# Optimization experiments

Measured on AMD Instinct MI355X. Metric: run time of the kernel, lower is better.

Reference implementation:

```python
import jax, jax.numpy as jnp
import numpy as np


def setup_inputs() -> dict:
    key = jax.random.key(0)
    k1, k2 = jax.random.split(key)
    enc_output = jax.random.normal(k1, (4, 4096, 1024), dtype=jnp.float32)
    dec_output = jax.random.normal(k2, (4, 4096, 1024), dtype=jnp.float32)
    return {"enc_output": enc_output, "dec_output": dec_output}


def reference(enc_output, dec_output):
    # a_t[b, e, t] = sum_d enc[b, e, d] * dec[b, t, d]   -> [B, T_enc, T_dec]
    a_t = jnp.einsum('bed,btd->bet', enc_output, dec_output)
    # softmax over dim=1 (the T_enc axis), no scaling, no mask (faithful to source)
    a_t = jax.nn.softmax(a_t, axis=1)
    # c_t[b, t, d] = sum_e a_t[b, e, t] * enc[b, e, d]   -> [B, T_dec, D]
    c_t = jnp.einsum('bet,bed->btd', a_t, enc_output)
    return c_t
```

## Files before the change

### kernel.cpp

```cpp
#include <hip/hip_runtime.h>
#include <hip/hip_fp16.h>

typedef _Float16 half_t;
typedef _Float16 f16x8 __attribute__((ext_vector_type(8)));
typedef _Float16 f16x4 __attribute__((ext_vector_type(4)));
typedef float f32x4 __attribute__((ext_vector_type(4)));
typedef __attribute__((address_space(3))) half_t* lds_p;

#define SEQ 4096
#define DDIM 1024
#define NBATCH 4

__device__ __forceinline__ void gload16(const half_t* g, half_t* l) {
  __builtin_amdgcn_global_load_lds((const __attribute__((address_space(1))) void*)g,
                                   (__attribute__((address_space(3))) void*)l, 16, 0, 0);
}

__device__ __forceinline__ f16x8 ds_read128(lds_p p) {
  f16x8 r;
  asm volatile("ds_read_b128 %0, %1" : "=v"(r) : "v"(p));
  return r;
}

__global__ __launch_bounds__(256) void conv_f16(const float* __restrict__ src,
                                                half_t* __restrict__ dst) {
  int i = blockIdx.x * 256 + threadIdx.x;
  float4 x = ((const float4*)src)[i];
  f16x4 o = {(half_t)x.x, (half_t)x.y, (half_t)x.z, (half_t)x.w};
  *(f16x4*)(dst + (size_t)i * 4) = o;
}

__global__ __launch_bounds__(256) void transconv_f16(const float* __restrict__ src,
                                                     half_t* __restrict__ dstF,
                                                     half_t* __restrict__ dstT) {
  __shared__ float tile[32][33];
  int b = blockIdx.z;
  int e0 = blockIdx.x * 32, d0 = blockIdx.y * 32;
  const float* s = src + (size_t)b * SEQ * DDIM;
  half_t* df = dstF + (size_t)b * SEQ * DDIM;
  half_t* dt = dstT + (size_t)b * DDIM * SEQ;
  int tx = threadIdx.x & 31, ty = threadIdx.x >> 5;
#pragma unroll
  for (int i = 0; i < 4; i++) {
    int e = e0 + ty + i * 8;
    float v = s[(size_t)e * DDIM + d0 + tx];
    tile[ty + i * 8][tx] = v;
    df[(size_t)e * DDIM + d0 + tx] = (half_t)v;
  }
  __syncthreads();
#pragma unroll
  for (int i = 0; i < 4; i++) {
    int d = d0 + ty + i * 8;
    dt[(size_t)d * SEQ + e0 + tx] = (half_t)tile[tx][ty + i * 8];
  }
}

#define TM 256
#define TN 256
#define TK 64

__global__ __launch_bounds__(512, 2) void gemm256_p2(const half_t* __restrict__ A,
                                                     const half_t* __restrict__ B,
                                                     float* __restrict__ C, int M, int N,
                                                     int K, int kc, long sA, long sB, long sC,
                                                     int atom) {
  A += (size_t)blockIdx.z * (size_t)sA;
  B += (size_t)blockIdx.z * (size_t)sB;
  C += (size_t)blockIdx.z * (size_t)sC;
  __shared__ __align__(16) half_t As[2][TM * TK];
  __shared__ __align__(16) half_t Bs[2][TN * TK];
  const int tid = threadIdx.x;
  const int wave = tid >> 6, lane = tid & 63;
  const int wm = (wave >> 2) * 128, wn = (wave & 3) * 64;
  const int mrow = lane & 15, quad = lane >> 4;

  f32x4 acc[8][4];
#pragma unroll
  for (int i = 0; i < 8; i++)
#pragma unroll
    for (int j = 0; j < 4; j++) acc[i][j] = {0.f, 0.f, 0.f, 0.f};

  const half_t* Ag = A + (size_t)(blockIdx.x * TM) * K;
  const half_t* Bg = B + (size_t)(blockIdx.y * TN) * K;
  lds_p As3 = (lds_p)&As[0][0];
  lds_p Bs3 = (lds_p)&Bs[0][0];

  auto stage = [&](int buf, int k0) {
#pragma unroll
    for (int i = 0; i < 4; i++) {
      int cid = i * 512 + tid;
      int row = cid >> 3, slot = cid & 7;
      int chunk = slot ^ (row & 7);
      gload16(Ag + (size_t)row * K + k0 + chunk * 8, &As[buf][row * TK + slot * 8]);
      gload16(Bg + (size_t)row * K + k0 + chunk * 8, &Bs[buf][row * TK + slot * 8]);
    }
  };

  const int nt = kc / TK;
  stage(0, 0);
  asm volatile("s_waitcnt vmcnt(0)" ::: "memory");
  __builtin_amdgcn_s_barrier();
  int cur = 0;
  for (int t = 0; t < nt; ++t) {
    if (t + 1 < nt) stage(cur ^ 1, (t + 1) * TK);
    lds_p Ab = As3 + cur * (TM * TK);
    lds_p Bb = Bs3 + cur * (TN * TK);
#pragma unroll
    for (int ks = 0; ks < 2; ks++) {
      f16x8 af[8], bf[4];
#pragma unroll
      for (int i = 0; i < 8; i++) {
        int ra = wm + i * 16 + mrow;
        int sa = (ks * 4 + quad) ^ (ra & 7);
        af[i] = ds_read128(Ab + ra * TK + sa * 8);
      }
#pragma unroll
      for (int j = 0; j < 4; j++) {
        int rb = wn + j * 16 + mrow;
        int sb = (ks * 4 + quad) ^ (rb & 7);
        bf[j] = ds_read128(Bb + rb * TK + sb * 8);
      }
      asm volatile("s_waitcnt lgkmcnt(0)" ::: "memory");
      __builtin_amdgcn_sched_barrier(0);
#pragma unroll
      for (int mi = 0; mi < 8; mi++)
#pragma unroll
        for (int ni = 0; ni < 4; ni++)
          acc[mi][ni] =
              __builtin_amdgcn_mfma_f32_16x16x32_f16(af[mi], bf[ni], acc[mi][ni], 0, 0, 0);
    }
    asm volatile("s_waitcnt vmcnt(0)" ::: "memory");
    __builtin_amdgcn_s_barrier();
    cur ^= 1;
  }
#pragma unroll
  for (int mi = 0; mi < 8; mi++) {
#pragma unroll
    for (int ni = 0; ni < 4; ni++) {
      int row0 = blockIdx.x * TM + wm + mi * 16 + quad * 4;
      int col = blockIdx.y * TN + wn + ni * 16 + mrow;
      float* Cp = C + (size_t)row0 * N + col;
      if (atom) {
#pragma unroll
        for (int r = 0; r < 4; r++) unsafeAtomicAdd(Cp + (size_t)r * N, acc[mi][ni][r]);
      } else {
#pragma unroll
        for (int r = 0; r < 4; r++) Cp[(size_t)r * N] = acc[mi][ni][r];
      }
    }
  }
}

__global__ __launch_bounds__(256) void softmax_rows(const float* __restrict__ S,
                                                    half_t* __restrict__ P) {
  const int row = blockIdx.x;
  const float4* Sr = (const float4*)(S + (size_t)row * SEQ);
  const int tid = threadIdx.x, lane = tid & 63, wave = tid >> 6;
  __shared__ float red[4];
  __shared__ float bc;
  float4 v[4];
  float m = -1e30f;
#pragma unroll
  for (int j = 0; j < 4; j++) {
    v[j] = Sr[tid + j * 256];
    m = fmaxf(m, fmaxf(fmaxf(v[j].x, v[j].y), fmaxf(v[j].z, v[j].w)));
  }
#pragma unroll
  for (int o = 32; o; o >>= 1) m = fmaxf(m, __shfl_xor(m, o));
  if (lane == 0) red[wave] = m;
  __syncthreads();
  if (tid == 0) bc = fmaxf(fmaxf(red[0], red[1]), fmaxf(red[2], red[3]));
  __syncthreads();
  m = bc;
  float s = 0.f;
#pragma unroll
  for (int j = 0; j < 4; j++) {
    v[j].x = __expf(v[j].x - m);
    v[j].y = __expf(v[j].y - m);
    v[j].z = __expf(v[j].z - m);
    v[j].w = __expf(v[j].w - m);
    s += v[j].x + v[j].y + v[j].z + v[j].w;
  }
#pragma unroll
  for (int o = 32; o; o >>= 1) s += __shfl_xor(s, o);
  __syncthreads();
  if (lane == 0) red[wave] = s;
  __syncthreads();
  if (tid == 0) bc = red[0] + red[1] + red[2] + red[3];
  __syncthreads();
  float r = 1.0f / bc;
  f16x4* Pr = (f16x4*)(P + (size_t)row * SEQ);
#pragma unroll
  for (int j = 0; j < 4; j++) {
    f16x4 o = {(half_t)(v[j].x * r), (half_t)(v[j].y * r), (half_t)(v[j].z * r),
               (half_t)(v[j].w * r)};
    Pr[tid + j * 256] = o;
  }
}

__global__ __launch_bounds__(256) void naive_attn(const float* __restrict__ enc,
                                                  const float* __restrict__ dec,
                                                  float* __restrict__ out) {
  const int b = blockIdx.y, t = blockIdx.x;
  const float* encb = enc + (size_t)b * SEQ * DDIM;
  const float* q = dec + ((size_t)b * SEQ + t) * DDIM;
  __shared__ float qs[DDIM];
  __shared__ float sc[SEQ];
  __shared__ float red[4];
  __shared__ float bc;
  const int tid = threadIdx.x, lane = tid & 63, wave = tid >> 6;
  for (int i = tid; i < DDIM; i += 256) qs[i] = q[i];
  __syncthreads();
  for (int e = tid; e < SEQ; e += 256) {
    const float* er = encb + (size_t)e * DDIM;
    float s = 0.f;
    for (int d = 0; d < DDIM; d += 4) {
      float4 ev = *(const float4*)(er + d);
      s += ev.x * qs[d] + ev.y * qs[d + 1] + ev.z * qs[d + 2] + ev.w * qs[d + 3];
    }
    sc[e] = s;
  }
  __syncthreads();
  float m = -1e30f;
  for (int e = tid; e < SEQ; e += 256) m = fmaxf(m, sc[e]);
#pragma unroll
  for (int o = 32; o; o >>= 1) m = fmaxf(m, __shfl_xor(m, o));
  if (lane == 0) red[wave] = m;
  __syncthreads();
  if (tid == 0) bc = fmaxf(fmaxf(red[0], red[1]), fmaxf(red[2], red[3]));
  __syncthreads();
  m = bc;
  float s = 0.f;
  for (int e = tid; e < SEQ; e += 256) {
    float p = __expf(sc[e] - m);
    sc[e] = p;
    s += p;
  }
#pragma unroll
  for (int o = 32; o; o >>= 1) s += __shfl_xor(s, o);
  __syncthreads();
  if (lane == 0) red[wave] = s;
  __syncthreads();
  if (tid == 0) bc = red[0] + red[1] + red[2] + red[3];
  __syncthreads();
  const float rinv = 1.0f / bc;
  const int d0 = tid * 4;
  float4 acc = {0.f, 0.f, 0.f, 0.f};
  for (int e = 0; e < SEQ; e++) {
    float p = sc[e];
    float4 ev = *(const float4*)(encb + (size_t)e * DDIM + d0);
    acc.x += p * ev.x;
    acc.y += p * ev.y;
    acc.z += p * ev.z;
    acc.w += p * ev.w;
  }
  float4* o4 = (float4*)(out + ((size_t)b * SEQ + t) * DDIM + d0);
  float4 res = {acc.x * rinv, acc.y * rinv, acc.z * rinv, acc.w * rinv};
  *o4 = res;
}

extern "C" void kernel_launch(void* const* d_in, const int* in_sizes, int n_in, void* d_out,
                              int out_size, void* d_ws, size_t ws_size, hipStream_t stream) {
  const float* enc = (const float*)d_in[0];
  const float* dec = (const float*)d_in[1];
  float* out = (float*)d_out;

  const size_t SZ_S = (size_t)SEQ * SEQ * 4;
  const size_t SZ_P = (size_t)SEQ * SEQ * 2;
  const size_t SZ_H = (size_t)NBATCH * SEQ * DDIM * 2;
  const size_t NEED = SZ_S + SZ_P + 3 * SZ_H;

  const int nconv = NBATCH * SEQ * DDIM / 4 / 256;

  if (ws_size >= NEED) {
    char* w = (char*)d_ws;
    float* S = (float*)w;
    half_t* P = (half_t*)(w + SZ_S);
    half_t* decF = (half_t*)(w + SZ_S + SZ_P);
    half_t* encF = (half_t*)(w + SZ_S + SZ_P + SZ_H);
    half_t* encT = (half_t*)(w + SZ_S + SZ_P + 2 * SZ_H);

    hipMemsetAsync(out, 0, (size_t)NBATCH * SEQ * DDIM * 4, stream);
    conv_f16<<<nconv, 256, 0, stream>>>(dec, decF);
    transconv_f16<<<dim3(SEQ / 32, DDIM / 32, NBATCH), 256, 0, stream>>>(enc, encF, encT);

    for (int b = 0; b < NBATCH; b++) {
      const size_t eo = (size_t)b * SEQ * DDIM;
      gemm256_p2<<<dim3(SEQ / TM, SEQ / TN, 1), 512, 0, stream>>>(
          decF + eo, encF + eo, S, SEQ, SEQ, DDIM, DDIM, 0, 0, 0, 0);
      softmax_rows<<<SEQ, 256, 0, stream>>>(S, P);
      gemm256_p2<<<dim3(SEQ / TM, DDIM / TN, 4), 512, 0, stream>>>(
          P, encT + (size_t)b * DDIM * SEQ, out + eo, SEQ, DDIM, SEQ, SEQ / 4, SEQ / 4,
          SEQ / 4, 0, 1);
    }
  } else {
    naive_attn<<<dim3(SEQ, NBATCH), 256, 0, stream>>>(enc, dec, out);
  }
}
```

Measured before the change: 682.1 us.

## Shrink GEMM N-tile to 128 and add triple-buffered LDS prefetch pipeline

The GEMM tile changes from 256x256 to 256x128 and the shared-memory staging goes from double to triple buffering. Loads for tile t+2 are issued while tile t is computed, with partial vmcnt waits so only the oldest stage has to land. The aim is to hide global-load latency and raise the number of blocks in the grid. In exchange, each wave does fewer MFMAs per byte loaded, which lowers data reuse. LDS use is 3x(32KB+16KB)=144KB per block, which may cut occupancy below the 2 blocks the launch bounds request.

```diff
diff --git a/kernel.cpp b/kernel.cpp
--- a/kernel.cpp
+++ b/kernel.cpp
@@ -56,29 +56,29 @@
 }
 
 #define TM 256
-#define TN 256
+#define TN 128
 #define TK 64
 
-__global__ __launch_bounds__(512, 2) void gemm256_p2(const half_t* __restrict__ A,
-                                                     const half_t* __restrict__ B,
-                                                     float* __restrict__ C, int M, int N,
-                                                     int K, int kc, long sA, long sB, long sC,
-                                                     int atom) {
+__global__ __launch_bounds__(512, 2) void gemm_p3(const half_t* __restrict__ A,
+                                                  const half_t* __restrict__ B,
+                                                  float* __restrict__ C, int M, int N, int K,
+                                                  int kc, long sA, long sB, long sC,
+                                                  int atom) {
   A += (size_t)blockIdx.z * (size_t)sA;
   B += (size_t)blockIdx.z * (size_t)sB;
   C += (size_t)blockIdx.z * (size_t)sC;
-  __shared__ __align__(16) half_t As[2][TM * TK];
-  __shared__ __align__(16) half_t Bs[2][TN * TK];
+  __shared__ __align__(16) half_t As[3][TM * TK];
+  __shared__ __align__(16) half_t Bs[3][TN * TK];
   const int tid = threadIdx.x;
   const int wave = tid >> 6, lane = tid & 63;
-  const int wm = (wave >> 2) * 128, wn = (wave & 3) * 64;
+  const int wm = (wave >> 2) * 128, wn = (wave & 3) * 32;
   const int mrow = lane & 15, quad = lane >> 4;
 
-  f32x4 acc[8][4];
+  f32x4 acc[8][2];
 #pragma unroll
   for (int i = 0; i < 8; i++)
 #pragma unroll
-    for (int j = 0; j < 4; j++) acc[i][j] = {0.f, 0.f, 0.f, 0.f};
+    for (int j = 0; j < 2; j++) acc[i][j] = {0.f, 0.f, 0.f, 0.f};
 
   const half_t* Ag = A + (size_t)(blockIdx.x * TM) * K;
   const half_t* Bg = B + (size_t)(blockIdx.y * TN) * K;
@@ -92,22 +92,34 @@
       int row = cid >> 3, slot = cid & 7;
       int chunk = slot ^ (row & 7);
       gload16(Ag + (size_t)row * K + k0 + chunk * 8, &As[buf][row * TK + slot * 8]);
+    }
+#pragma unroll
+    for (int i = 0; i < 2; i++) {
+      int cid = i * 512 + tid;
+      int row = cid >> 3, slot = cid & 7;
+      int chunk = slot ^ (row & 7);
       gload16(Bg + (size_t)row * K + k0 + chunk * 8, &Bs[buf][row * TK + slot * 8]);
     }
   };
 
   const int nt = kc / TK;
   stage(0, 0);
-  asm volatile("s_waitcnt vmcnt(0)" ::: "memory");
+  if (nt > 1) {
+    stage(1, TK);
+    asm volatile("s_waitcnt vmcnt(6)" ::: "memory");
+  } else {
+    asm volatile("s_waitcnt vmcnt(0)" ::: "memory");
+  }
   __builtin_amdgcn_s_barrier();
-  int cur = 0;
+
+  int ib0 = 0, ib1 = 1, ib2 = 2;
   for (int t = 0; t < nt; ++t) {
-    if (t + 1 < nt) stage(cur ^ 1, (t + 1) * TK);
-    lds_p Ab = As3 + cur * (TM * TK);
-    lds_p Bb = Bs3 + cur * (TN * TK);
+    if (t + 2 < nt) stage(ib2, (t + 2) * TK);
+    lds_p Ab = As3 + ib0 * (TM * TK);
+    lds_p Bb = Bs3 + ib0 * (TN * TK);
 #pragma unroll
     for (int ks = 0; ks < 2; ks++) {
-      f16x8 af[8], bf[4];
+      f16x8 af[8], bf[2];
 #pragma unroll
       for (int i = 0; i < 8; i++) {
         int ra = wm + i * 16 + mrow;
@@ -115,7 +127,7 @@
         af[i] = ds_read128(Ab + ra * TK + sa * 8);
       }
 #pragma unroll
-      for (int j = 0; j < 4; j++) {
+      for (int j = 0; j < 2; j++) {
         int rb = wn + j * 16 + mrow;
         int sb = (ks * 4 + quad) ^ (rb & 7);
         bf[j] = ds_read128(Bb + rb * TK + sb * 8);
@@ -125,18 +137,26 @@
 #pragma unroll
       for (int mi = 0; mi < 8; mi++)
 #pragma unroll
-        for (int ni = 0; ni < 4; ni++)
+        for (int ni = 0; ni < 2; ni++)
           acc[mi][ni] =
               __builtin_amdgcn_mfma_f32_16x16x32_f16(af[mi], bf[ni], acc[mi][ni], 0, 0, 0);
     }
-    asm volatile("s_waitcnt vmcnt(0)" ::: "memory");
-    __builtin_amdgcn_s_barrier();
-    cur ^= 1;
+    if (t + 1 < nt) {
+      if (t + 2 < nt)
+        asm volatile("s_waitcnt vmcnt(6)" ::: "memory");
+      else
+        asm volatile("s_waitcnt vmcnt(0)" ::: "memory");
+      __builtin_amdgcn_s_barrier();
+    }
+    int tmp = ib0;
+    ib0 = ib1;
+    ib1 = ib2;
+    ib2 = tmp;
   }
 #pragma unroll
   for (int mi = 0; mi < 8; mi++) {
 #pragma unroll
-    for (int ni = 0; ni < 4; ni++) {
+    for (int ni = 0; ni < 2; ni++) {
       int row0 = blockIdx.x * TM + wm + mi * 16 + quad * 4;
       int col = blockIdx.y * TN + wn + ni * 16 + mrow;
       float* Cp = C + (size_t)row0 * N + col;
@@ -286,10 +306,10 @@
 
     for (int b = 0; b < NBATCH; b++) {
       const size_t eo = (size_t)b * SEQ * DDIM;
-      gemm256_p2<<<dim3(SEQ / TM, SEQ / TN, 1), 512, 0, stream>>>(
+      gemm_p3<<<dim3(SEQ / TM, SEQ / TN, 1), 512, 0, stream>>>(
           decF + eo, encF + eo, S, SEQ, SEQ, DDIM, DDIM, 0, 0, 0, 0);
       softmax_rows<<<SEQ, 256, 0, stream>>>(S, P);
-      gemm256_p2<<<dim3(SEQ / TM, DDIM / TN, 4), 512, 0, stream>>>(
+      gemm_p3<<<dim3(SEQ / TM, DDIM / TN, 4), 512, 0, stream>>>(
           P, encT + (size_t)b * DDIM * SEQ, out + eo, SEQ, DDIM, SEQ, SEQ / 4, SEQ / 4,
           SEQ / 4, 0, 1);
     }
```

After: 747.9 us. 1.1x slower.

## Rewrite GEMM main loop as eight-phase ping-pong schedule with interleaved loads

Applied to the files above, without the earlier changes.

Replaces the simple double-buffered GEMM loop with an 8-phase schedule per two K-tiles. Each phase issues a partial global-to-LDS stage, a partial LDS fragment read and a quarter of the MFMA work, separated by barriers and s_setprio. The goal is to overlap global loads and LDS reads with matrix ops and to keep the two co-resident blocks alternating on the matrix units. It adds many more barriers and hand-tuned vmcnt waits, which could hurt if the phase counts are wrong.

```diff
diff --git a/kernel.cpp b/kernel.cpp
--- a/kernel.cpp
+++ b/kernel.cpp
@@ -59,20 +59,45 @@
 #define TN 256
 #define TK 64
 
-__global__ __launch_bounds__(512, 2) void gemm256_p2(const half_t* __restrict__ A,
-                                                     const half_t* __restrict__ B,
-                                                     float* __restrict__ C, int M, int N,
-                                                     int K, int kc, long sA, long sB, long sC,
-                                                     int atom) {
+#define SYNC_PRE()                                     \
+  do {                                                 \
+    __builtin_amdgcn_s_barrier();                      \
+    __builtin_amdgcn_sched_barrier(0);                 \
+    asm volatile("s_waitcnt lgkmcnt(0)" ::: "memory"); \
+    __builtin_amdgcn_sched_barrier(0);                 \
+    __builtin_amdgcn_s_setprio(1);                     \
+  } while (0)
+#define SYNC_POST()                    \
+  do {                                 \
+    __builtin_amdgcn_s_setprio(0);     \
+    __builtin_amdgcn_s_barrier();      \
+    __builtin_amdgcn_sched_barrier(0); \
+  } while (0)
+#define QMMA(qm, qn, FB)                                                             \
+  {                                                                                  \
+    _Pragma("unroll") for (int j = 0; j < 4; j++) {                                  \
+      _Pragma("unroll") for (int jn = 0; jn < 2; jn++) {                             \
+        acc[(qm)*4 + j][(qn)*2 + jn] = __builtin_amdgcn_mfma_f32_16x16x32_f16(       \
+            fa[j][0], FB[jn][0], acc[(qm)*4 + j][(qn)*2 + jn], 0, 0, 0);             \
+        acc[(qm)*4 + j][(qn)*2 + jn] = __builtin_amdgcn_mfma_f32_16x16x32_f16(       \
+            fa[j][1], FB[jn][1], acc[(qm)*4 + j][(qn)*2 + jn], 0, 0, 0);             \
+      }                                                                              \
+    }                                                                                \
+  }
+
+__global__ __launch_bounds__(512, 2) void gemm8p(const half_t* __restrict__ A,
+                                                 const half_t* __restrict__ B,
+                                                 float* __restrict__ C, int M, int N, int K,
+                                                 int kc, long sA, long sB, long sC, int atom) {
   A += (size_t)blockIdx.z * (size_t)sA;
   B += (size_t)blockIdx.z * (size_t)sB;
   C += (size_t)blockIdx.z * (size_t)sC;
-  __shared__ __align__(16) half_t As[2][TM * TK];
-  __shared__ __align__(16) half_t Bs[2][TN * TK];
+  __shared__ __align__(16) half_t Ls[65536];
   const int tid = threadIdx.x;
   const int wave = tid >> 6, lane = tid & 63;
   const int wm = (wave >> 2) * 128, wn = (wave & 3) * 64;
   const int mrow = lane & 15, quad = lane >> 4;
+  const int sw0 = quad ^ (mrow & 7);
 
   f32x4 acc[8][4];
 #pragma unroll
@@ -82,64 +107,137 @@
 
   const half_t* Ag = A + (size_t)(blockIdx.x * TM) * K;
   const half_t* Bg = B + (size_t)(blockIdx.y * TN) * K;
-  lds_p As3 = (lds_p)&As[0][0];
-  lds_p Bs3 = (lds_p)&Bs[0][0];
-
-  auto stage = [&](int buf, int k0) {
-#pragma unroll
-    for (int i = 0; i < 4; i++) {
-      int cid = i * 512 + tid;
-      int row = cid >> 3, slot = cid & 7;
-      int chunk = slot ^ (row & 7);
-      gload16(Ag + (size_t)row * K + k0 + chunk * 8, &As[buf][row * TK + slot * 8]);
-      gload16(Bg + (size_t)row * K + k0 + chunk * 8, &Bs[buf][row * TK + slot * 8]);
-    }
+  lds_p L3 = (lds_p)&Ls[0];
+
+  const int row0 = tid >> 3, slot = tid & 7;
+  const int chunk = slot ^ (row0 & 7);
+  const size_t gOffA0 = (size_t)row0 * K + chunk * 8;
+  const size_t gOffA1 = gOffA0 + (size_t)64 * K;
+  const int lOff0 = row0 * 64 + slot * 8, lOff1 = lOff0 + 4096;
+
+  auto stA = [&](int tt, int h) {
+    size_t go = (size_t)tt * TK + (size_t)h * 128 * K;
+    int lo = (tt & 1) * 16384 + h * 8192;
+    gload16(Ag + go + gOffA0, &Ls[lo + lOff0]);
+    gload16(Ag + go + gOffA1, &Ls[lo + lOff1]);
   };
+  auto stB = [&](int tt, int h) {
+    size_t go = (size_t)tt * TK + (size_t)h * 128 * K;
+    int lo = 32768 + (tt & 1) * 16384 + h * 8192;
+    gload16(Bg + go + gOffA0, &Ls[lo + lOff0]);
+    gload16(Bg + go + gOffA1, &Ls[lo + lOff1]);
+  };
+  auto rdA = [&](int b, int m, int ks) {
+    return ds_read128(L3 + b * 16384 + (wm + m * 16 + mrow) * 64 + ((ks * 4) ^ sw0) * 8);
+  };
+  auto rdB = [&](int b, int n, int ks) {
+    return ds_read128(L3 + 32768 + b * 16384 + (wn + n * 16 + mrow) * 64 +
+                      ((ks * 4) ^ sw0) * 8);
+  };
 
   const int nt = kc / TK;
-  stage(0, 0);
-  asm volatile("s_waitcnt vmcnt(0)" ::: "memory");
+  const int niter = nt / 2;
+  stB(0, 0);
+  stB(0, 1);
+  stA(0, 0);
+  stA(0, 1);
+  stB(1, 0);
+  stB(1, 1);
+  asm volatile("s_waitcnt vmcnt(4)" ::: "memory");
   __builtin_amdgcn_s_barrier();
-  int cur = 0;
-  for (int t = 0; t < nt; ++t) {
-    if (t + 1 < nt) stage(cur ^ 1, (t + 1) * TK);
-    lds_p Ab = As3 + cur * (TM * TK);
-    lds_p Bb = Bs3 + cur * (TN * TK);
-#pragma unroll
-    for (int ks = 0; ks < 2; ks++) {
-      f16x8 af[8], bf[4];
-#pragma unroll
-      for (int i = 0; i < 8; i++) {
-        int ra = wm + i * 16 + mrow;
-        int sa = (ks * 4 + quad) ^ (ra & 7);
-        af[i] = ds_read128(Ab + ra * TK + sa * 8);
-      }
-#pragma unroll
-      for (int j = 0; j < 4; j++) {
-        int rb = wn + j * 16 + mrow;
-        int sb = (ks * 4 + quad) ^ (rb & 7);
-        bf[j] = ds_read128(Bb + rb * TK + sb * 8);
-      }
-      asm volatile("s_waitcnt lgkmcnt(0)" ::: "memory");
-      __builtin_amdgcn_sched_barrier(0);
-#pragma unroll
-      for (int mi = 0; mi < 8; mi++)
-#pragma unroll
-        for (int ni = 0; ni < 4; ni++)
-          acc[mi][ni] =
-              __builtin_amdgcn_mfma_f32_16x16x32_f16(af[mi], bf[ni], acc[mi][ni], 0, 0, 0);
-    }
-    asm volatile("s_waitcnt vmcnt(0)" ::: "memory");
-    __builtin_amdgcn_s_barrier();
-    cur ^= 1;
+  __builtin_amdgcn_sched_barrier(0);
+
+  f16x8 fa[4][2], fb0[2][2], fb1[2][2];
+  for (int i = 0; i < niter; ++i) {
+    const int t0 = 2 * i, t1 = t0 + 1;
+#pragma unroll
+    for (int j = 0; j < 4; j++) {
+      fa[j][0] = rdA(0, j, 0);
+      fa[j][1] = rdA(0, j, 1);
+    }
+#pragma unroll
+    for (int jn = 0; jn < 2; jn++) {
+      fb0[jn][0] = rdB(0, jn, 0);
+      fb0[jn][1] = rdB(0, jn, 1);
+    }
+    stA(t1, 0);
+    SYNC_PRE();
+    QMMA(0, 0, fb0);
+    SYNC_POST();
+#pragma unroll
+    for (int jn = 0; jn < 2; jn++) {
+      fb1[jn][0] = rdB(0, 2 + jn, 0);
+      fb1[jn][1] = rdB(0, 2 + jn, 1);
+    }
+    stA(t1, 1);
+    SYNC_PRE();
+    QMMA(0, 1, fb1);
+    SYNC_POST();
+#pragma unroll
+    for (int j = 0; j < 4; j++) {
+      fa[j][0] = rdA(0, 4 + j, 0);
+      fa[j][1] = rdA(0, 4 + j, 1);
+    }
+    if (t0 + 2 < nt) stB(t0 + 2, 0);
+    SYNC_PRE();
+    QMMA(1, 1, fb1);
+    SYNC_POST();
+    if (t0 + 2 < nt) {
+      stB(t0 + 2, 1);
+      asm volatile("s_waitcnt vmcnt(4)" ::: "memory");
+    } else {
+      asm volatile("s_waitcnt vmcnt(0)" ::: "memory");
+    }
+    SYNC_PRE();
+    QMMA(1, 0, fb0);
+    SYNC_POST();
+#pragma unroll
+    for (int j = 0; j < 4; j++) {
+      fa[j][0] = rdA(1, j, 0);
+      fa[j][1] = rdA(1, j, 1);
+    }
+#pragma unroll
+    for (int jn = 0; jn < 2; jn++) {
+      fb0[jn][0] = rdB(1, jn, 0);
+      fb0[jn][1] = rdB(1, jn, 1);
+    }
+    if (t0 + 2 < nt) stA(t0 + 2, 0);
+    SYNC_PRE();
+    QMMA(0, 0, fb0);
+    SYNC_POST();
+#pragma unroll
+    for (int jn = 0; jn < 2; jn++) {
+      fb1[jn][0] = rdB(1, 2 + jn, 0);
+      fb1[jn][1] = rdB(1, 2 + jn, 1);
+    }
+    if (t0 + 2 < nt) stA(t0 + 2, 1);
+    SYNC_PRE();
+    QMMA(0, 1, fb1);
+    SYNC_POST();
+#pragma unroll
+    for (int j = 0; j < 4; j++) {
+      fa[j][0] = rdA(1, 4 + j, 0);
+      fa[j][1] = rdA(1, 4 + j, 1);
+    }
+    if (t1 + 2 < nt) stB(t1 + 2, 0);
+    SYNC_PRE();
+    QMMA(1, 1, fb1);
+    SYNC_POST();
+    if (t1 + 2 < nt) {
+      stB(t1 + 2, 1);
+      asm volatile("s_waitcnt vmcnt(4)" ::: "memory");
+    }
+    SYNC_PRE();
+    QMMA(1, 0, fb0);
+    SYNC_POST();
   }
 #pragma unroll
   for (int mi = 0; mi < 8; mi++) {
 #pragma unroll
     for (int ni = 0; ni < 4; ni++) {
-      int row0 = blockIdx.x * TM + wm + mi * 16 + quad * 4;
+      int row0_ = blockIdx.x * TM + wm + mi * 16 + quad * 4;
       int col = blockIdx.y * TN + wn + ni * 16 + mrow;
-      float* Cp = C + (size_t)row0 * N + col;
+      float* Cp = C + (size_t)row0_ * N + col;
       if (atom) {
 #pragma unroll
         for (int r = 0; r < 4; r++) unsafeAtomicAdd(Cp + (size_t)r * N, acc[mi][ni][r]);
@@ -286,10 +384,10 @@
 
     for (int b = 0; b < NBATCH; b++) {
       const size_t eo = (size_t)b * SEQ * DDIM;
-      gemm256_p2<<<dim3(SEQ / TM, SEQ / TN, 1), 512, 0, stream>>>(
-          decF + eo, encF + eo, S, SEQ, SEQ, DDIM, DDIM, 0, 0, 0, 0);
+      gemm8p<<<dim3(SEQ / TM, SEQ / TN, 1), 512, 0, stream>>>(decF + eo, encF + eo, S, SEQ,
+                                                              SEQ, DDIM, DDIM, 0, 0, 0, 0);
       softmax_rows<<<SEQ, 256, 0, stream>>>(S, P);
-      gemm256_p2<<<dim3(SEQ / TM, DDIM / TN, 4), 512, 0, stream>>>(
+      gemm8p<<<dim3(SEQ / TM, DDIM / TN, 4), 512, 0, stream>>>(
           P, encT + (size_t)b * DDIM * SEQ, out + eo, SEQ, DDIM, SEQ, SEQ / 4, SEQ / 4,
           SEQ / 4, 0, 1);
     }
```

New measurement: 694.1 us. No clear change (+1.7%).
